# Kernel tuning notes

Hardware: AMD Instinct MI355X
Metric: run time of the kernel (lower is better)

## Reference

```python
import jax, jax.numpy as jnp
import numpy as np

HEADS, DIM_HEAD, BLOCK, EPS = 16, 64, 16, 1e-8


def _hattn(x, w_qkv, w_out, b_out):
    b, n, dim = x.shape
    h, dh, bsz = HEADS, DIM_HEAD, BLOCK
    scale = dh ** -0.5
    # n is a power of two, so the module's pad-to-pow2 step is a no-op.
    qkv = x @ w_qkv  # [b, n, 3*h*dh]
    q, k, v = jnp.split(qkv, 3, axis=-1)

    def to_heads(t):  # [b, n, h*dh] -> [(b h), n, dh]
        return t.reshape(b, n, h, dh).transpose(0, 2, 1, 3).reshape(b * h, n, dh)

    q, k, v = to_heads(q) * scale, to_heads(k), to_heads(v)

    num_levels = int(np.log2(n // bsz)) - 1
    levels = [(q, k, v)]
    for _ in range(num_levels):  # coarsen: mean-pool q,k; sum-pool v (mask=None path)
        q = q.reshape(b * h, -1, 2, dh).mean(axis=2)
        k = k.reshape(b * h, -1, 2, dh).mean(axis=2)
        v = v.reshape(b * h, -1, 2, dh).sum(axis=2)
        levels.append((q, k, v))

    def flip_blocks(t):  # swap adjacent blocks along the block axis: [B, nb, z, d]
        B, nb, z, d = t.shape
        return t.reshape(B, nb // 2, 2, z, d)[:, :, ::-1].reshape(B, nb, z, d)

    Ys = []
    last = len(levels) - 1
    for ind, (ql, kl, vl) in enumerate(reversed(levels)):  # coarsest -> finest
        B, N, d = ql.shape
        qb = ql.reshape(B, N // bsz, bsz, d)
        kb = vb = None
        kb = kl.reshape(B, N // bsz, bsz, d)
        vb = vl.reshape(B, N // bsz, bsz, d)
        if ind != last:  # off-diagonal pairing at coarse levels
            kb, vb = flip_blocks(kb), flip_blocks(vb)
        S = jnp.einsum('bnid,bnjd->bnij', qb, kb)
        S = S - S.max(axis=-1, keepdims=True)
        A = jnp.exp(S)
        y = jnp.einsum('bnij,bnjd->bnid', A, vb)
        Ys.append((y.reshape(B, N, d), A.sum(-1).reshape(B, N)))

    Y, Asum = Ys[0]
    for y_l, a_l in Ys[1:]:  # upsample-and-accumulate across levels
        Y = jnp.repeat(Y, 2, axis=1) + y_l
        Asum = jnp.repeat(Asum, 2, axis=1) + a_l

    out = Y / (Asum + EPS)[..., None]  # [(b h), n, dh]
    out = out.reshape(b, h, n, dh).transpose(0, 2, 1, 3).reshape(b, n, h * dh)
    return out @ w_out + b_out


def setup_inputs() -> dict:
    key = jax.random.key(0)
    k1, k2, k3 = jax.random.split(key, 3)
    b, n, dim = 4, 8192, 1024
    inner = HEADS * DIM_HEAD
    x = jax.random.normal(k1, (b, n, dim), dtype=jnp.float32)
    w_qkv = jax.random.normal(k2, (dim, inner * 3), dtype=jnp.float32) * 0.02
    w_out = jax.random.normal(k3, (inner, dim), dtype=jnp.float32) * 0.02
    b_out = jnp.zeros((dim,), dtype=jnp.float32)
    return {"x": x, "w_qkv": w_qkv, "w_out": w_out, "b_out": b_out}


def reference(x, w_qkv, w_out, b_out):
    return _hattn(x, w_qkv, w_out, b_out)
```

## Files before the change

### kernel.cpp

```cpp
#include <hip/hip_runtime.h>

typedef unsigned short u16;
typedef unsigned int u32;
typedef __bf16 bf16x8 __attribute__((ext_vector_type(8)));
typedef float f32x4 __attribute__((ext_vector_type(4)));

__device__ inline float bf2f(u16 u) { u32 x = ((u32)u) << 16; return __uint_as_float(x); }
__device__ inline u16 f2bf(float f) {
  u32 x = __float_as_uint(f);
  u32 r = (x + 0x7FFFu + ((x >> 16) & 1u)) >> 16;
  return (u16)r;
}
__device__ inline u32 pack2(float lo, float hi) {
  return (u32)f2bf(lo) | ((u32)f2bf(hi) << 16);
}

__global__ __launch_bounds__(256) void cast_bf16(const float* __restrict__ s,
                                                 u16* __restrict__ d, int n4) {
  const float4* s4 = (const float4*)s;
  u32* d2 = (u32*)d;
  int i = blockIdx.x * 256 + threadIdx.x;
  int stride = gridDim.x * 256;
  for (; i < n4; i += stride) {
    float4 f = s4[i];
    d2[2 * i]     = pack2(f.x, f.y);
    d2[2 * i + 1] = pack2(f.z, f.w);
  }
}

__global__ __launch_bounds__(256) void transpose_cast(const float* __restrict__ src,
                                                      u16* __restrict__ dst, int R, int C) {
  __shared__ float tile[32][33];
  int bx = blockIdx.x, by = blockIdx.y;
  int tx = threadIdx.x & 31, ty = threadIdx.x >> 5;
  for (int rr = ty; rr < 32; rr += 8)
    tile[rr][tx] = src[(size_t)(by * 32 + rr) * C + bx * 32 + tx];
  __syncthreads();
  for (int rr = ty; rr < 32; rr += 8)
    dst[(size_t)(bx * 32 + rr) * R + by * 32 + tx] = f2bf(tile[tx][rr]);
}

#define MFMAQ(AF, BF, MO, NO)                                                     \
  _Pragma("unroll") for (int mf = 0; mf < 4; ++mf)                                \
  _Pragma("unroll") for (int nf = 0; nf < 2; ++nf)                                \
  _Pragma("unroll") for (int kq = 0; kq < 2; ++kq)                                \
    acc[(MO) + mf][(NO) + nf] = __builtin_amdgcn_mfma_f32_16x16x32_bf16(          \
        AF[mf][kq], BF[nf][kq], acc[(MO) + mf][(NO) + nf], 0, 0, 0);

#define PH_OPEN12                                                                 \
  asm volatile("s_waitcnt lgkmcnt(8)" ::: "memory");                              \
  __builtin_amdgcn_s_barrier();                                                   \
  asm volatile("s_waitcnt lgkmcnt(0)" ::: "memory");                              \
  __builtin_amdgcn_sched_barrier(0);                                              \
  __builtin_amdgcn_s_setprio(1);

#define PH_OPEN                                                                   \
  __builtin_amdgcn_s_barrier();                                                   \
  asm volatile("s_waitcnt lgkmcnt(0)" ::: "memory");                              \
  __builtin_amdgcn_sched_barrier(0);                                              \
  __builtin_amdgcn_s_setprio(1);

#define PH_CLOSE                                                                  \
  __builtin_amdgcn_s_setprio(0);                                                  \
  __builtin_amdgcn_s_barrier();                                                   \
  __builtin_amdgcn_sched_barrier(0);

#define PH_CLOSE_VM                                                               \
  __builtin_amdgcn_s_setprio(0);                                                  \
  asm volatile("s_waitcnt vmcnt(4)" ::: "memory");                                \
  __builtin_amdgcn_s_barrier();                                                   \
  __builtin_amdgcn_sched_barrier(0);

template <int EPI>
__global__ __launch_bounds__(512, 2) void gemm8p(
    const u16* __restrict__ A, const u16* __restrict__ Bt, int M, int N, int K, int NB,
    u16* __restrict__ q0, u16* __restrict__ k0, u16* __restrict__ v0,
    u16* __restrict__ q4, u16* __restrict__ k4, u16* __restrict__ v4,
    float* __restrict__ out, const float* __restrict__ bias) {
  __shared__ u16 lds[2][2][16384];
  const int tid = threadIdx.x;
  const int lane = tid & 63;
  const int wave = tid >> 6;
  const int wm = wave >> 2, wn = wave & 3;
  const int lr = lane & 15, lg = lane >> 4;

  const int nwg = gridDim.x;
  const int bid = blockIdx.x;
  const int swz = (bid & 7) * (nwg >> 3) + (bid >> 3);
  const int m0 = (swz / NB) * 256;
  const int n0 = (swz % NB) * 256;
  const int NT = K >> 6;
  const int NI = NT >> 1;

  auto stage_half = [&](int buf, int ht, int kt_) {
    const u16* src = (ht < 2) ? A : Bt;
    const int r0 = (ht < 2) ? m0 : n0;
    u16* ldsop = &lds[buf][ht >> 1][0];
#pragma unroll
    for (int ii = 0; ii < 2; ++ii) {
      int c2 = ((ht & 1) * 2 + ii) * 512 + tid;
      int row = c2 >> 3, ps = c2 & 7;
      int ks = ps ^ (row & 7);
      const u16* g = src + (size_t)(r0 + row) * K + kt_ + ks * 8;
      char* l = (char*)ldsop + (size_t)((((ht & 1) * 2 + ii) * 512 + (tid & ~63)) * 16);
      __builtin_amdgcn_global_load_lds((const __attribute__((address_space(1))) void*)g,
                                       (__attribute__((address_space(3))) void*)l, 16, 0, 0);
    }
  };
  auto rdA = [&](int c, int mf, int kq) -> bf16x8 {
    int rl = wm * 128 + mf * 16 + lr;
    int sl = (kq * 4 + lg) ^ (rl & 7);
    return *(const bf16x8*)(&lds[c][0][rl * 64 + sl * 8]);
  };
  auto rdB = [&](int c, int nf, int kq) -> bf16x8 {
    int rl = wn * 64 + nf * 16 + lr;
    int sl = (kq * 4 + lg) ^ (rl & 7);
    return *(const bf16x8*)(&lds[c][1][rl * 64 + sl * 8]);
  };

  f32x4 acc[8][4];
#pragma unroll
  for (int mf = 0; mf < 8; ++mf)
#pragma unroll
    for (int nf = 0; nf < 4; ++nf) acc[mf][nf] = f32x4{0.f, 0.f, 0.f, 0.f};

  stage_half(0, 2, 0); stage_half(0, 3, 0); stage_half(0, 0, 0); stage_half(0, 1, 0);
  stage_half(1, 2, 64); stage_half(1, 3, 64);
  asm volatile("s_waitcnt vmcnt(4)" ::: "memory");
  __builtin_amdgcn_s_barrier();
  __builtin_amdgcn_sched_barrier(0);

  bf16x8 afA[4][2], afB[4][2], bA[2][2], bB[2][2];
  for (int it = 0; it < NI; ++it) {
    const int kO  = (2 * it + 1) << 6;
    const int t2  = 2 * it + 2, t3 = 2 * it + 3;
    const int kE2 = ((t2 < NT) ? t2 : NT - 1) << 6;
    const int kO2 = ((t3 < NT) ? t3 : NT - 1) << 6;

#pragma unroll
    for (int mf = 0; mf < 4; ++mf) { afA[mf][0] = rdA(0, mf, 0); afA[mf][1] = rdA(0, mf, 1); }
#pragma unroll
    for (int nf = 0; nf < 2; ++nf) { bA[nf][0] = rdB(0, nf, 0); bA[nf][1] = rdB(0, nf, 1); }
    stage_half(1, 0, kO);
    PH_OPEN12 MFMAQ(afA, bA, 0, 0) PH_CLOSE
#pragma unroll
    for (int nf = 0; nf < 2; ++nf) { bB[nf][0] = rdB(0, 2 + nf, 0); bB[nf][1] = rdB(0, 2 + nf, 1); }
    stage_half(1, 1, kO);
    PH_OPEN MFMAQ(afA, bB, 0, 2) PH_CLOSE
#pragma unroll
    for (int mf = 0; mf < 4; ++mf) { afB[mf][0] = rdA(0, 4 + mf, 0); afB[mf][1] = rdA(0, 4 + mf, 1); }
    stage_half(0, 2, kE2);
    PH_OPEN MFMAQ(afB, bB, 4, 2) PH_CLOSE
    stage_half(0, 3, kE2);
    PH_OPEN MFMAQ(afB, bA, 4, 0) PH_CLOSE_VM
#pragma unroll
    for (int mf = 0; mf < 4; ++mf) { afA[mf][0] = rdA(1, mf, 0); afA[mf][1] = rdA(1, mf, 1); }
#pragma unroll
    for (int nf = 0; nf < 2; ++nf) { bA[nf][0] = rdB(1, nf, 0); bA[nf][1] = rdB(1, nf, 1); }
    stage_half(0, 0, kE2);
    PH_OPEN12 MFMAQ(afA, bA, 0, 0) PH_CLOSE
#pragma unroll
    for (int nf = 0; nf < 2; ++nf) { bB[nf][0] = rdB(1, 2 + nf, 0); bB[nf][1] = rdB(1, 2 + nf, 1); }
    stage_half(0, 1, kE2);
    PH_OPEN MFMAQ(afA, bB, 0, 2) PH_CLOSE
#pragma unroll
    for (int mf = 0; mf < 4; ++mf) { afB[mf][0] = rdA(1, 4 + mf, 0); afB[mf][1] = rdA(1, 4 + mf, 1); }
    stage_half(1, 2, kO2);
    PH_OPEN MFMAQ(afB, bB, 4, 2) PH_CLOSE
    stage_half(1, 3, kO2);
    PH_OPEN MFMAQ(afB, bA, 4, 0) PH_CLOSE_VM
  }
  asm volatile("s_waitcnt vmcnt(0)" ::: "memory");

#pragma unroll
  for (int mf = 0; mf < 8; ++mf) {
#pragma unroll
    for (int nf = 0; nf < 4; ++nf) {
      int col = n0 + wn * 64 + nf * 16 + lr;
      if (EPI == 0) {
        int p = col >> 10, cc = col & 1023;
        int h = cc >> 6, d = cc & 63;
        u16* dst = (p == 0) ? q0 : (p == 1) ? k0 : v0;
        float sc = (p == 0) ? 0.125f : 1.0f;
#pragma unroll
        for (int jj = 0; jj < 4; ++jj) {
          int row = m0 + wm * 128 + mf * 16 + lg * 4 + jj;
          int b = row >> 13, nn = row & 8191;
          dst[((size_t)((b << 4) + h) * 8192 + nn) * 64 + d] = f2bf(acc[mf][nf][jj] * sc);
        }
        float s4 = acc[mf][nf][0] + acc[mf][nf][1] + acc[mf][nf][2] + acc[mf][nf][3];
        s4 += __shfl_xor(s4, 16);
        s4 += __shfl_xor(s4, 32);
        if (lane < 16) {
          int row = m0 + wm * 128 + mf * 16;
          int b = row >> 13, n4 = (row & 8191) >> 4;
          u16* dst4 = (p == 0) ? q4 : (p == 1) ? k4 : v4;
          float val = (p == 2) ? s4 : s4 * 0.0625f;
          if (p == 0) val *= 0.125f;
          dst4[((size_t)((b << 4) + h) * 512 + n4) * 64 + d] = f2bf(val);
        }
      } else {
        float bv = bias[col];
#pragma unroll
        for (int jj = 0; jj < 4; ++jj) {
          int row = m0 + wm * 128 + mf * 16 + lg * 4 + jj;
          out[(size_t)row * N + col] = acc[mf][nf][jj] + bv;
        }
      }
    }
  }
}

__global__ __launch_bounds__(256) void pool_level(
    const u16* __restrict__ qs, const u16* __restrict__ ks, const u16* __restrict__ vs,
    u16* __restrict__ qd, u16* __restrict__ kd, u16* __restrict__ vd, int P) {
  int t = blockIdx.x * 256 + threadIdx.x;
  if (t >= P) return;
  int a = blockIdx.y;
  const u32* s = (const u32*)(a == 0 ? qs : a == 1 ? ks : vs);
  u32* d = (u32*)(a == 0 ? qd : a == 1 ? kd : vd);
  int row = t >> 5, dp = t & 31;
  u32 u0 = s[(size_t)(2 * row) * 32 + dp];
  u32 u1 = s[(size_t)(2 * row + 1) * 32 + dp];
  float x0 = bf2f((u16)u0), x1 = bf2f((u16)(u0 >> 16));
  float y0 = bf2f((u16)u1), y1 = bf2f((u16)(u1 >> 16));
  float sc = (a == 2) ? 1.0f : 0.5f;
  d[t] = pack2((x0 + y0) * sc, (x1 + y1) * sc);
}

__global__ __launch_bounds__(256) void hattn_level(
    const u16* __restrict__ q, const u16* __restrict__ k, const u16* __restrict__ v,
    const float* __restrict__ pY, const float* __restrict__ pA,
    float* __restrict__ Ycur, float* __restrict__ Acur, int N) {
  __shared__ float qs[16][68], ks[16][68], vs[16][68];
  __shared__ float As[16][17];
  const int tid = threadIdx.x;
  const int jb = blockIdx.x;
  const int Bi = blockIdx.y;
  const int jk = jb ^ 1;
  const u32* qg = (const u32*)(q + ((size_t)Bi * N + jb * 16) * 64);
  const u32* kg = (const u32*)(k + ((size_t)Bi * N + jk * 16) * 64);
  const u32* vg = (const u32*)(v + ((size_t)Bi * N + jk * 16) * 64);
#pragma unroll
  for (int u = tid; u < 512; u += 256) {
    int row = u >> 5, dp = (u & 31) * 2;
    u32 a = qg[u]; qs[row][dp] = bf2f((u16)a); qs[row][dp + 1] = bf2f((u16)(a >> 16));
    u32 b = kg[u]; ks[row][dp] = bf2f((u16)b); ks[row][dp + 1] = bf2f((u16)(b >> 16));
    u32 c = vg[u]; vs[row][dp] = bf2f((u16)c); vs[row][dp + 1] = bf2f((u16)(c >> 16));
  }
  __syncthreads();
  const int i = tid >> 4, j = tid & 15;
  float s = 0.f;
  const float4* qv = (const float4*)&qs[i][0];
  const float4* kv = (const float4*)&ks[j][0];
#pragma unroll
  for (int d4 = 0; d4 < 16; ++d4) {
    float4 a = qv[d4], b = kv[d4];
    s += a.x * b.x + a.y * b.y + a.z * b.z + a.w * b.w;
  }
  float mx = s;
#pragma unroll
  for (int off = 8; off; off >>= 1) mx = fmaxf(mx, __shfl_xor(mx, off, 16));
  float aexp = __expf(s - mx);
  float asum = aexp;
#pragma unroll
  for (int off = 8; off; off >>= 1) asum += __shfl_xor(asum, off, 16);
  As[i][j] = aexp;
  __syncthreads();
  float y0 = 0, y1 = 0, y2 = 0, y3 = 0;
  const int d0 = j * 4;
#pragma unroll
  for (int jj = 0; jj < 16; ++jj) {
    float av = As[i][jj];
    const float4 vv = *(const float4*)&vs[jj][d0];
    y0 += av * vv.x; y1 += av * vv.y; y2 += av * vv.z; y3 += av * vv.w;
  }
  const int nf = jb * 16 + i;
  float at = asum;
  if (pY) {
    const float* py = pY + ((size_t)Bi * (N >> 1) + (nf >> 1)) * 64 + d0;
    y0 += py[0]; y1 += py[1]; y2 += py[2]; y3 += py[3];
    at += pA[(size_t)Bi * (N >> 1) + (nf >> 1)];
  }
  float* yo = Ycur + ((size_t)Bi * N + nf) * 64 + d0;
  yo[0] = y0; yo[1] = y1; yo[2] = y2; yo[3] = y3;
  if (j == 0) Acur[(size_t)Bi * N + nf] = at;
}

union F8 { u32 w[4]; bf16x8 v; };

__device__ inline void acc_row8(const u16* p, float* a) {
  const u32* qw = (const u32*)p;
#pragma unroll
  for (int m = 0; m < 4; ++m) {
    u32 u = qw[m];
    a[2 * m]     += bf2f((u16)u);
    a[2 * m + 1] += bf2f((u16)(u >> 16));
  }
}
__device__ inline bf16x8 mk8(const float* a, float s) {
  F8 f;
#pragma unroll
  for (int m = 0; m < 4; ++m) f.w[m] = pack2(a[2 * m] * s, a[2 * m + 1] * s);
  return f.v;
}
__device__ inline bf16x8 pool_frag(const u16* arr, int row0, int cnt, int slotq, float scale) {
  float a[8] = {0, 0, 0, 0, 0, 0, 0, 0};
  for (int m = 0; m < cnt; ++m) {
    int r = row0 + m;
    acc_row8(arr + r * 64 + ((slotq ^ (r & 7)) * 8), a);
  }
  return mk8(a, scale);
}
__device__ inline bf16x8 rd_frag(const u16* arr, int r, int slotq) {
  return *(const bf16x8*)(arr + r * 64 + ((slotq ^ (r & 7)) * 8));
}
template <int LVL>
__device__ inline bf16x8 vt_frag(const u16* Vt, int c, int rbase) {
  float a[8] = {0, 0, 0, 0, 0, 0, 0, 0};
  const u32* p = (const u32*)(Vt + c * 264 + rbase);
#pragma unroll
  for (int g = 0; g < (1 << LVL); ++g) {
#pragma unroll
    for (int m = 0; m < 4; ++m) {
      u32 u = p[g * 4 + m];
      int t = g * 8 + 2 * m;
      a[t >> LVL]       += bf2f((u16)u);
      a[(t + 1) >> LVL] += bf2f((u16)(u >> 16));
    }
  }
  return mk8(a, 1.0f);
}

__device__ inline bf16x8 qk_softmax(bf16x8 ka0, bf16x8 ka1, bf16x8 qb0, bf16x8 qb1,
                                    int lane, float* asum_out) {
  f32x4 s = {0.f, 0.f, 0.f, 0.f};
  s = __builtin_amdgcn_mfma_f32_16x16x32_bf16(ka0, qb0, s, 0, 0, 0);
  s = __builtin_amdgcn_mfma_f32_16x16x32_bf16(ka1, qb1, s, 0, 0, 0);
  float mx = fmaxf(fmaxf(s[0], s[1]), fmaxf(s[2], s[3]));
  mx = fmaxf(mx, __shfl_xor(mx, 32));
  mx = fmaxf(mx, __shfl_xor(mx, 16));
  float p0 = __expf(s[0] - mx), p1 = __expf(s[1] - mx);
  float p2 = __expf(s[2] - mx), p3 = __expf(s[3] - mx);
  float as = p0 + p1 + p2 + p3;
  as += __shfl_xor(as, 32);
  as += __shfl_xor(as, 16);
  *asum_out = as;
  u32 pk01 = pack2(p0, p1), pk23 = pack2(p2, p3);
  int jq = lane & 15, lg = lane >> 4;
  int a1 = ((((lg * 2) * 16) + jq) & 63) << 2;
  int a2 = ((((lg * 2 + 1) * 16) + jq) & 63) << 2;
  F8 f;
  f.w[0] = (u32)__builtin_amdgcn_ds_bpermute(a1, (int)pk01);
  f.w[1] = (u32)__builtin_amdgcn_ds_bpermute(a1, (int)pk23);
  f.w[2] = (u32)__builtin_amdgcn_ds_bpermute(a2, (int)pk01);
  f.w[3] = (u32)__builtin_amdgcn_ds_bpermute(a2, (int)pk23);
  if (lg >= 2) { f.w[0] = 0; f.w[1] = 0; f.w[2] = 0; f.w[3] = 0; }
  return f.v;
}

__global__ __launch_bounds__(512, 1) void attn_fine(
    const u16* __restrict__ q, const u16* __restrict__ k, const u16* __restrict__ v,
    const float* __restrict__ Y4, const float* __restrict__ A4,
    u16* __restrict__ outA) {
  __shared__ u16 Qs[16384];
  __shared__ u16 Ks[16384];
  __shared__ u16 Vt[16896];
  __shared__ float Yc1[128][68];
  __shared__ float Yc2[64][68];
  __shared__ float Yc3[32][68];
  __shared__ float SUMc[224];
  const int tid = threadIdx.x;
  const int lane = tid & 63;
  const int wv = tid >> 6;
  const int j = lane & 15, lg = lane >> 4;
  const int ci = blockIdx.x, Bi = blockIdx.y;
  const size_t gbase = ((size_t)Bi * 8192 + (size_t)ci * 256) * 64;

#pragma unroll
  for (int it = 0; it < 4; ++it) {
    int sidx = it * 512 + tid;
    int row = sidx >> 3, ps = sidx & 7;
    int ks_ = ps ^ (row & 7);
    const u16* gq = q + gbase + (size_t)row * 64 + ks_ * 8;
    const u16* gk = k + gbase + (size_t)row * 64 + ks_ * 8;
    char* lq = (char*)Qs + (size_t)(it * 512 + (tid & ~63)) * 16;
    char* lk = (char*)Ks + (size_t)(it * 512 + (tid & ~63)) * 16;
    __builtin_amdgcn_global_load_lds((const __attribute__((address_space(1))) void*)gq,
                                     (__attribute__((address_space(3))) void*)lq, 16, 0, 0);
    __builtin_amdgcn_global_load_lds((const __attribute__((address_space(1))) void*)gk,
                                     (__attribute__((address_space(3))) void*)lk, 16, 0, 0);
  }
  {
    const uint4* gv = (const uint4*)(v + gbase);
    u32* Vt32 = (u32*)Vt;
#pragma unroll
    for (int it = 0; it < 2; ++it) {
      int i = it * 512 + tid;
      int r2 = i >> 3, cg = i & 7, c0 = cg * 8;
      uint4 a = gv[(size_t)(2 * r2) * 8 + cg];
      uint4 b = gv[(size_t)(2 * r2 + 1) * 8 + cg];
      const u16* pa = (const u16*)&a;
      const u16* pb = (const u16*)&b;
#pragma unroll
      for (int m = 0; m < 8; ++m)
        Vt32[(c0 + m) * 132 + r2] = (u32)pa[m] | ((u32)pb[m] << 16);
    }
  }
  __syncthreads();

  {
    int kb = wv ^ 1;
    bf16x8 ka0 = pool_frag(Ks, kb * 32 + 2 * j, 2, lg, 0.5f);
    bf16x8 ka1 = pool_frag(Ks, kb * 32 + 2 * j, 2, 4 + lg, 0.5f);
    bf16x8 qb0 = pool_frag(Qs, wv * 32 + 2 * j, 2, lg, 0.5f);
    bf16x8 qb1 = pool_frag(Qs, wv * 32 + 2 * j, 2, 4 + lg, 0.5f);
    float as;
    bf16x8 pa = qk_softmax(ka0, ka1, qb0, qb1, lane, &as);
    if (lg == 0) SUMc[wv * 16 + j] = as;
    int rb = kb * 32 + (lg & 1) * 16;
    f32x4 acc[4];
#pragma unroll
    for (int ch = 0; ch < 4; ++ch) {
      bf16x8 vb = vt_frag<1>(Vt, ch * 16 + j, rb);
      acc[ch] = __builtin_amdgcn_mfma_f32_16x16x32_bf16(pa, vb, f32x4{0.f,0.f,0.f,0.f}, 0, 0, 0);
    }
#pragma unroll
    for (int ch = 0; ch < 4; ++ch)
#pragma unroll
      for (int jj = 0; jj < 4; ++jj)
        Yc1[wv * 16 + lg * 4 + jj][ch * 16 + j] = acc[ch][jj];
  }
  if (wv < 4) {
    int kb = wv ^ 1;
    bf16x8 ka0 = pool_frag(Ks, kb * 64 + 4 * j, 4, lg, 0.25f);
    bf16x8 ka1 = pool_frag(Ks, kb * 64 + 4 * j, 4, 4 + lg, 0.25f);
    bf16x8 qb0 = pool_frag(Qs, wv * 64 + 4 * j, 4, lg, 0.25f);
    bf16x8 qb1 = pool_frag(Qs, wv * 64 + 4 * j, 4, 4 + lg, 0.25f);
    float as;
    bf16x8 pa = qk_softmax(ka0, ka1, qb0, qb1, lane, &as);
    if (lg == 0) SUMc[128 + wv * 16 + j] = as;
    int rb = kb * 64 + (lg & 1) * 32;
    f32x4 acc[4];
#pragma unroll
    for (int ch = 0; ch < 4; ++ch) {
      bf16x8 vb = vt_frag<2>(Vt, ch * 16 + j, rb);
      acc[ch] = __builtin_amdgcn_mfma_f32_16x16x32_bf16(pa, vb, f32x4{0.f,0.f,0.f,0.f}, 0, 0, 0);
    }
#pragma unroll
    for (int ch = 0; ch < 4; ++ch)
#pragma unroll
      for (int jj = 0; jj < 4; ++jj)
        Yc2[wv * 16 + lg * 4 + jj][ch * 16 + j] = acc[ch][jj];
  }
  if (wv >= 6) {
    int w3 = wv - 6;
    int kb = w3 ^ 1;
    bf16x8 ka0 = pool_frag(Ks, kb * 128 + 8 * j, 8, lg, 0.125f);
    bf16x8 ka1 = pool_frag(Ks, kb * 128 + 8 * j, 8, 4 + lg, 0.125f);
    bf16x8 qb0 = pool_frag(Qs, w3 * 128 + 8 * j, 8, lg, 0.125f);
    bf16x8 qb1 = pool_frag(Qs, w3 * 128 + 8 * j, 8, 4 + lg, 0.125f);
    float as;
    bf16x8 pa = qk_softmax(ka0, ka1, qb0, qb1, lane, &as);
    if (lg == 0) SUMc[192 + w3 * 16 + j] = as;
    int rb = kb * 128 + (lg & 1) * 64;
    f32x4 acc[4];
#pragma unroll
    for (int ch = 0; ch < 4; ++ch) {
      bf16x8 vb = vt_frag<3>(Vt, ch * 16 + j, rb);
      acc[ch] = __builtin_amdgcn_mfma_f32_16x16x32_bf16(pa, vb, f32x4{0.f,0.f,0.f,0.f}, 0, 0, 0);
    }
#pragma unroll
    for (int ch = 0; ch < 4; ++ch)
#pragma unroll
      for (int jj = 0; jj < 4; ++jj)
        Yc3[w3 * 16 + lg * 4 + jj][ch * 16 + j] = acc[ch][jj];
  }
  __syncthreads();

  const int batch = Bi >> 4, h = Bi & 15;
#pragma unroll
  for (int bb = 0; bb < 2; ++bb) {
    int b = wv * 2 + bb;
    bf16x8 ka0 = rd_frag(Ks, b * 16 + j, lg);
    bf16x8 ka1 = rd_frag(Ks, b * 16 + j, 4 + lg);
    bf16x8 qb0 = rd_frag(Qs, b * 16 + j, lg);
    bf16x8 qb1 = rd_frag(Qs, b * 16 + j, 4 + lg);
    float as;
    bf16x8 pa = qk_softmax(ka0, ka1, qb0, qb1, lane, &as);
    float av[4];
#pragma unroll
    for (int jj = 0; jj < 4; ++jj)
      av[jj] = __int_as_float(__builtin_amdgcn_ds_bpermute((lg * 4 + jj) << 2,
                                                           __float_as_int(as)));
    int rb = b * 16 + (lg & 1) * 8;
    f32x4 acc[4];
#pragma unroll
    for (int ch = 0; ch < 4; ++ch) {
      bf16x8 vb = *(const bf16x8*)(Vt + (ch * 16 + j) * 264 + rb);
      acc[ch] = __builtin_amdgcn_mfma_f32_16x16x32_bf16(pa, vb, f32x4{0.f,0.f,0.f,0.f}, 0, 0, 0);
    }
    const size_t Y4row = (size_t)Bi * 512 + ci * 16 + b;
    float a4 = A4[Y4row];
    float y4v[4];
#pragma unroll
    for (int ch = 0; ch < 4; ++ch) y4v[ch] = Y4[Y4row * 64 + ch * 16 + j];
#pragma unroll
    for (int jj = 0; jj < 4; ++jj) {
      int r0 = b * 16 + lg * 4 + jj;
      float at = av[jj] + SUMc[r0 >> 1] + SUMc[128 + (r0 >> 2)] + SUMc[192 + (r0 >> 3)] + a4;
      float inv = 1.0f / (at + 1e-8f);
      size_t n = (size_t)ci * 256 + r0;
      u16* orow = outA + ((size_t)batch * 8192 + n) * 1024 + h * 64 + j;
#pragma unroll
      for (int ch = 0; ch < 4; ++ch) {
        float yt = acc[ch][jj] + Yc1[r0 >> 1][ch * 16 + j] + Yc2[r0 >> 2][ch * 16 + j] +
                   Yc3[r0 >> 3][ch * 16 + j] + y4v[ch];
        orow[ch * 16] = f2bf(yt * inv);
      }
    }
  }
}

extern "C" void kernel_launch(void* const* d_in, const int* in_sizes, int n_in,
                              void* d_out, int out_size, void* d_ws, size_t ws_size,
                              hipStream_t stream) {
  const float* x = (const float*)d_in[0];
  const float* w_qkv = (const float*)d_in[1];
  const float* w_out = (const float*)d_in[2];
  const float* b_out = (const float*)d_in[3];
  float* out = (float*)d_out;

  char* ws = (char*)d_ws;
  size_t off = 0;
  auto alloc = [&](size_t bytes) -> char* {
    char* p = ws + off;
    off += (bytes + 255) & ~(size_t)255;
    return p;
  };
  u16* xb = (u16*)alloc(33554432ull * 2);
  u16* wqkvT = (u16*)alloc(3072ull * 1024 * 2);
  u16* woutT = (u16*)alloc(1024ull * 1024 * 2);
  u16* q0 = (u16*)alloc(67108864ull);
  u16* k0 = (u16*)alloc(67108864ull);
  u16* v0 = (u16*)alloc(67108864ull);
  u16* qc = (u16*)alloc(8388608ull);
  u16* kc = (u16*)alloc(8388608ull);
  u16* vc = (u16*)alloc(8388608ull);
  float* Ybuf[2];
  Ybuf[0] = (float*)alloc(8388608ull);
  Ybuf[1] = (float*)alloc(8388608ull);
  float* Abuf[2];
  Abuf[0] = (float*)alloc(131072ull);
  Abuf[1] = (float*)alloc(131072ull);
  (void)ws_size; (void)in_sizes; (void)n_in; (void)out_size;

  cast_bf16<<<2048, 256, 0, stream>>>(x, xb, 33554432 / 4);
  transpose_cast<<<dim3(3072 / 32, 1024 / 32), 256, 0, stream>>>(w_qkv, wqkvT, 1024, 3072);
  transpose_cast<<<dim3(1024 / 32, 1024 / 32), 256, 0, stream>>>(w_out, woutT, 1024, 1024);

  const u16 *ql[9], *kl[9], *vl[9];
  ql[0] = q0; kl[0] = k0; vl[0] = v0;
  size_t co = 0;
  for (int l = 4; l <= 8; ++l) {
    ql[l] = qc + co; kl[l] = kc + co; vl[l] = vc + co;
    co += (size_t)64 * (8192 >> l) * 64;
  }

  gemm8p<0><<<1536, 512, 0, stream>>>(xb, wqkvT, 32768, 3072, 1024, 12,
                                      q0, k0, v0,
                                      (u16*)ql[4], (u16*)kl[4], (u16*)vl[4],
                                      nullptr, nullptr);

  for (int l = 5; l <= 8; ++l) {
    int Nl = 8192 >> l;
    int P = 64 * Nl * 32;
    pool_level<<<dim3((P + 255) / 256, 3), 256, 0, stream>>>(
        ql[l - 1], kl[l - 1], vl[l - 1], (u16*)ql[l], (u16*)kl[l], (u16*)vl[l], P);
  }
  for (int l = 8; l >= 4; --l) {
    int Nl = 8192 >> l;
    const float* pY = (l == 8) ? nullptr : Ybuf[(l + 1) & 1];
    const float* pA = (l == 8) ? nullptr : Abuf[(l + 1) & 1];
    hattn_level<<<dim3(Nl / 16, 64), 256, 0, stream>>>(
        ql[l], kl[l], vl[l], pY, pA, Ybuf[l & 1], Abuf[l & 1], Nl);
  }
  attn_fine<<<dim3(32, 64), 512, 0, stream>>>(q0, k0, v0, Ybuf[0], Abuf[0], xb);

  gemm8p<1><<<512, 512, 0, stream>>>(xb, woutT, 32768, 1024, 1024, 4,
                                     nullptr, nullptr, nullptr,
                                     nullptr, nullptr, nullptr, out, b_out);
}
```

Measured before the change: 473.1 us.

## Triple-buffer A tiles in GEMM and fuse coarse hierarchy into two launches

The GEMM main loop now processes one k-tile per iteration, with a three-deep LDS ring for A and a double buffer for B, and waits on vmcnt(8) so more loads stay in flight. The per-level pooling and coarse attention launches become one pooling kernel that builds every level from level 4, and one coarse-attention kernel that writes per-level outputs. attn_fine sums these outputs directly instead of reading an upsampled cascade. This removes serialized small launches and intermediate accumulation, at the cost of more LDS and extra reads in attn_fine.

```diff
diff --git a/kernel.cpp b/kernel.cpp
--- a/kernel.cpp
+++ b/kernel.cpp
@@ -65,9 +65,9 @@
   __builtin_amdgcn_s_barrier();                                                   \
   __builtin_amdgcn_sched_barrier(0);
 
-#define PH_CLOSE_VM                                                               \
+#define PH_CLOSE_VM8                                                              \
   __builtin_amdgcn_s_setprio(0);                                                  \
-  asm volatile("s_waitcnt vmcnt(4)" ::: "memory");                                \
+  asm volatile("s_waitcnt vmcnt(8)" ::: "memory");                                \
   __builtin_amdgcn_s_barrier();                                                   \
   __builtin_amdgcn_sched_barrier(0);
 
@@ -77,7 +77,8 @@
     u16* __restrict__ q0, u16* __restrict__ k0, u16* __restrict__ v0,
     u16* __restrict__ q4, u16* __restrict__ k4, u16* __restrict__ v4,
     float* __restrict__ out, const float* __restrict__ bias) {
-  __shared__ u16 lds[2][2][16384];
+  __shared__ u16 ldsA[3][16384];
+  __shared__ u16 ldsB[2][16384];
   const int tid = threadIdx.x;
   const int lane = tid & 63;
   const int wave = tid >> 6;
@@ -90,32 +91,28 @@
   const int m0 = (swz / NB) * 256;
   const int n0 = (swz % NB) * 256;
   const int NT = K >> 6;
-  const int NI = NT >> 1;
-
-  auto stage_half = [&](int buf, int ht, int kt_) {
-    const u16* src = (ht < 2) ? A : Bt;
-    const int r0 = (ht < 2) ? m0 : n0;
-    u16* ldsop = &lds[buf][ht >> 1][0];
+
+  auto stage_half = [&](u16* ldsop, const u16* src, int r0, int hb, int kt_) {
 #pragma unroll
     for (int ii = 0; ii < 2; ++ii) {
-      int c2 = ((ht & 1) * 2 + ii) * 512 + tid;
+      int c2 = (hb * 2 + ii) * 512 + tid;
       int row = c2 >> 3, ps = c2 & 7;
       int ks = ps ^ (row & 7);
       const u16* g = src + (size_t)(r0 + row) * K + kt_ + ks * 8;
-      char* l = (char*)ldsop + (size_t)((((ht & 1) * 2 + ii) * 512 + (tid & ~63)) * 16);
+      char* l = (char*)ldsop + (size_t)(((hb * 2 + ii) * 512 + (tid & ~63)) * 16);
       __builtin_amdgcn_global_load_lds((const __attribute__((address_space(1))) void*)g,
                                        (__attribute__((address_space(3))) void*)l, 16, 0, 0);
     }
   };
-  auto rdA = [&](int c, int mf, int kq) -> bf16x8 {
+  auto rdA = [&](const u16* Ab, int mf, int kq) -> bf16x8 {
     int rl = wm * 128 + mf * 16 + lr;
     int sl = (kq * 4 + lg) ^ (rl & 7);
-    return *(const bf16x8*)(&lds[c][0][rl * 64 + sl * 8]);
+    return *(const bf16x8*)(Ab + rl * 64 + sl * 8);
   };
-  auto rdB = [&](int c, int nf, int kq) -> bf16x8 {
+  auto rdB = [&](const u16* Bb, int nf, int kq) -> bf16x8 {
     int rl = wn * 64 + nf * 16 + lr;
     int sl = (kq * 4 + lg) ^ (rl & 7);
-    return *(const bf16x8*)(&lds[c][1][rl * 64 + sl * 8]);
+    return *(const bf16x8*)(Bb + rl * 64 + sl * 8);
   };
 
   f32x4 acc[8][4];
@@ -124,51 +121,39 @@
 #pragma unroll
     for (int nf = 0; nf < 4; ++nf) acc[mf][nf] = f32x4{0.f, 0.f, 0.f, 0.f};
 
-  stage_half(0, 2, 0); stage_half(0, 3, 0); stage_half(0, 0, 0); stage_half(0, 1, 0);
-  stage_half(1, 2, 64); stage_half(1, 3, 64);
-  asm volatile("s_waitcnt vmcnt(4)" ::: "memory");
+  stage_half(ldsA[0], A, m0, 0, 0); stage_half(ldsA[0], A, m0, 1, 0);
+  stage_half(ldsB[0], Bt, n0, 0, 0); stage_half(ldsB[0], Bt, n0, 1, 0);
+  const int k1 = ((NT > 1) ? 1 : 0) << 6;
+  stage_half(ldsA[1], A, m0, 0, k1); stage_half(ldsA[1], A, m0, 1, k1);
+  stage_half(ldsB[1], Bt, n0, 0, k1); stage_half(ldsB[1], Bt, n0, 1, k1);
+  asm volatile("s_waitcnt vmcnt(8)" ::: "memory");
   __builtin_amdgcn_s_barrier();
   __builtin_amdgcn_sched_barrier(0);
 
-  bf16x8 afA[4][2], afB[4][2], bA[2][2], bB[2][2];
-  for (int it = 0; it < NI; ++it) {
-    const int kO  = (2 * it + 1) << 6;
-    const int t2  = 2 * it + 2, t3 = 2 * it + 3;
-    const int kE2 = ((t2 < NT) ? t2 : NT - 1) << 6;
-    const int kO2 = ((t3 < NT) ? t3 : NT - 1) << 6;
-
-#pragma unroll
-    for (int mf = 0; mf < 4; ++mf) { afA[mf][0] = rdA(0, mf, 0); afA[mf][1] = rdA(0, mf, 1); }
-#pragma unroll
-    for (int nf = 0; nf < 2; ++nf) { bA[nf][0] = rdB(0, nf, 0); bA[nf][1] = rdB(0, nf, 1); }
-    stage_half(1, 0, kO);
+  for (int t = 0; t < NT; ++t) {
+    const u16* Ab = ldsA[t % 3];
+    const u16* Bb = ldsB[t & 1];
+    u16* A2 = ldsA[(t + 2) % 3];
+    u16* B2 = ldsB[t & 1];
+    const int k2 = (((t + 2) < NT) ? (t + 2) : (NT - 1)) << 6;
+
+    bf16x8 afA[4][2], afB[4][2], bA[2][2], bB[2][2];
+#pragma unroll
+    for (int mf = 0; mf < 4; ++mf) { afA[mf][0] = rdA(Ab, mf, 0); afA[mf][1] = rdA(Ab, mf, 1); }
+#pragma unroll
+    for (int nf = 0; nf < 2; ++nf) { bA[nf][0] = rdB(Bb, nf, 0); bA[nf][1] = rdB(Bb, nf, 1); }
+    stage_half(A2, A, m0, 0, k2);
     PH_OPEN12 MFMAQ(afA, bA, 0, 0) PH_CLOSE
 #pragma unroll
-    for (int nf = 0; nf < 2; ++nf) { bB[nf][0] = rdB(0, 2 + nf, 0); bB[nf][1] = rdB(0, 2 + nf, 1); }
-    stage_half(1, 1, kO);
+    for (int nf = 0; nf < 2; ++nf) { bB[nf][0] = rdB(Bb, 2 + nf, 0); bB[nf][1] = rdB(Bb, 2 + nf, 1); }
+    stage_half(A2, A, m0, 1, k2);
     PH_OPEN MFMAQ(afA, bB, 0, 2) PH_CLOSE
 #pragma unroll
-    for (int mf = 0; mf < 4; ++mf) { afB[mf][0] = rdA(0, 4 + mf, 0); afB[mf][1] = rdA(0, 4 + mf, 1); }
-    stage_half(0, 2, kE2);
+    for (int mf = 0; mf < 4; ++mf) { afB[mf][0] = rdA(Ab, 4 + mf, 0); afB[mf][1] = rdA(Ab, 4 + mf, 1); }
+    stage_half(B2, Bt, n0, 0, k2);
     PH_OPEN MFMAQ(afB, bB, 4, 2) PH_CLOSE
-    stage_half(0, 3, kE2);
-    PH_OPEN MFMAQ(afB, bA, 4, 0) PH_CLOSE_VM
-#pragma unroll
-    for (int mf = 0; mf < 4; ++mf) { afA[mf][0] = rdA(1, mf, 0); afA[mf][1] = rdA(1, mf, 1); }
-#pragma unroll
-    for (int nf = 0; nf < 2; ++nf) { bA[nf][0] = rdB(1, nf, 0); bA[nf][1] = rdB(1, nf, 1); }
-    stage_half(0, 0, kE2);
-    PH_OPEN12 MFMAQ(afA, bA, 0, 0) PH_CLOSE
-#pragma unroll
-    for (int nf = 0; nf < 2; ++nf) { bB[nf][0] = rdB(1, 2 + nf, 0); bB[nf][1] = rdB(1, 2 + nf, 1); }
-    stage_half(0, 1, kE2);
-    PH_OPEN MFMAQ(afA, bB, 0, 2) PH_CLOSE
-#pragma unroll
-    for (int mf = 0; mf < 4; ++mf) { afB[mf][0] = rdA(1, 4 + mf, 0); afB[mf][1] = rdA(1, 4 + mf, 1); }
-    stage_half(1, 2, kO2);
-    PH_OPEN MFMAQ(afB, bB, 4, 2) PH_CLOSE
-    stage_half(1, 3, kO2);
-    PH_OPEN MFMAQ(afB, bA, 4, 0) PH_CLOSE_VM
+    stage_half(B2, Bt, n0, 1, k2);
+    PH_OPEN MFMAQ(afB, bA, 4, 0) PH_CLOSE_VM8
   }
   asm volatile("s_waitcnt vmcnt(0)" ::: "memory");
 
@@ -211,36 +196,57 @@
   }
 }
 
-__global__ __launch_bounds__(256) void pool_level(
-    const u16* __restrict__ qs, const u16* __restrict__ ks, const u16* __restrict__ vs,
-    u16* __restrict__ qd, u16* __restrict__ kd, u16* __restrict__ vd, int P) {
+__global__ __launch_bounds__(256) void pool_all4(
+    const u16* __restrict__ q4, const u16* __restrict__ k4, const u16* __restrict__ v4,
+    u16* __restrict__ qd, u16* __restrict__ kd, u16* __restrict__ vd) {
   int t = blockIdx.x * 256 + threadIdx.x;
-  if (t >= P) return;
-  int a = blockIdx.y;
-  const u32* s = (const u32*)(a == 0 ? qs : a == 1 ? ks : vs);
-  u32* d = (u32*)(a == 0 ? qd : a == 1 ? kd : vd);
-  int row = t >> 5, dp = t & 31;
-  u32 u0 = s[(size_t)(2 * row) * 32 + dp];
-  u32 u1 = s[(size_t)(2 * row + 1) * 32 + dp];
-  float x0 = bf2f((u16)u0), x1 = bf2f((u16)(u0 >> 16));
-  float y0 = bf2f((u16)u1), y1 = bf2f((u16)(u1 >> 16));
-  float sc = (a == 2) ? 1.0f : 0.5f;
-  d[t] = pack2((x0 + y0) * sc, (x1 + y1) * sc);
-}
-
-__global__ __launch_bounds__(256) void hattn_level(
-    const u16* __restrict__ q, const u16* __restrict__ k, const u16* __restrict__ v,
-    const float* __restrict__ pY, const float* __restrict__ pA,
-    float* __restrict__ Ycur, float* __restrict__ Acur, int N) {
+  if (t >= 983040) return;
+  int arr = blockIdx.y;
+  int col = t & 31;
+  int rr = t >> 5;
+  int Bi = rr / 480;
+  int r = rr % 480;
+  int base, w, Nl;
+  if (r < 256)      { base = 0;   w = 2;  Nl = 256; }
+  else if (r < 384) { base = 256; w = 4;  Nl = 128; r -= 256; }
+  else if (r < 448) { base = 384; w = 8;  Nl = 64;  r -= 384; }
+  else              { base = 448; w = 16; Nl = 32;  r -= 448; }
+  const u32* s = (const u32*)(arr == 0 ? q4 : arr == 1 ? k4 : v4);
+  const u32* src = s + ((size_t)Bi * 512 + (size_t)r * w) * 32 + col;
+  float lo = 0, hi = 0;
+  for (int m = 0; m < w; ++m) {
+    u32 u = src[(size_t)m * 32];
+    lo += bf2f((u16)u); hi += bf2f((u16)(u >> 16));
+  }
+  float sc = (arr == 2) ? 1.0f : (1.0f / (float)w);
+  u32* d = (u32*)(arr == 0 ? qd : arr == 1 ? kd : vd);
+  d[(size_t)2048 * base + ((size_t)Bi * Nl + r) * 32 + col] = pack2(lo * sc, hi * sc);
+}
+
+__global__ __launch_bounds__(256) void hattn_coarse(
+    const u16* __restrict__ q4, const u16* __restrict__ k4, const u16* __restrict__ v4,
+    const u16* __restrict__ qc, const u16* __restrict__ kc, const u16* __restrict__ vc,
+    float* __restrict__ ylvl, float* __restrict__ alvl) {
   __shared__ float qs[16][68], ks[16][68], vs[16][68];
   __shared__ float As[16][17];
+  const int bx = blockIdx.x, Bi = blockIdx.y;
+  int lvl, jb;
+  if (bx < 32)      { lvl = 0; jb = bx; }
+  else if (bx < 48) { lvl = 1; jb = bx - 32; }
+  else if (bx < 56) { lvl = 2; jb = bx - 48; }
+  else if (bx < 60) { lvl = 3; jb = bx - 56; }
+  else              { lvl = 4; jb = bx - 60; }
+  const int N = 512 >> lvl;
+  const int srcb[5] = {0, 0, 256, 384, 448};
+  const int offr[5] = {0, 512, 768, 896, 960};
+  const u16* qp = (lvl == 0) ? q4 : qc + (size_t)4096 * srcb[lvl];
+  const u16* kp = (lvl == 0) ? k4 : kc + (size_t)4096 * srcb[lvl];
+  const u16* vp = (lvl == 0) ? v4 : vc + (size_t)4096 * srcb[lvl];
   const int tid = threadIdx.x;
-  const int jb = blockIdx.x;
-  const int Bi = blockIdx.y;
   const int jk = jb ^ 1;
-  const u32* qg = (const u32*)(q + ((size_t)Bi * N + jb * 16) * 64);
-  const u32* kg = (const u32*)(k + ((size_t)Bi * N + jk * 16) * 64);
-  const u32* vg = (const u32*)(v + ((size_t)Bi * N + jk * 16) * 64);
+  const u32* qg = (const u32*)(qp + ((size_t)Bi * N + jb * 16) * 64);
+  const u32* kg = (const u32*)(kp + ((size_t)Bi * N + jk * 16) * 64);
+  const u32* vg = (const u32*)(vp + ((size_t)Bi * N + jk * 16) * 64);
 #pragma unroll
   for (int u = tid; u < 512; u += 256) {
     int row = u >> 5, dp = (u & 31) * 2;
@@ -276,15 +282,9 @@
     y0 += av * vv.x; y1 += av * vv.y; y2 += av * vv.z; y3 += av * vv.w;
   }
   const int nf = jb * 16 + i;
-  float at = asum;
-  if (pY) {
-    const float* py = pY + ((size_t)Bi * (N >> 1) + (nf >> 1)) * 64 + d0;
-    y0 += py[0]; y1 += py[1]; y2 += py[2]; y3 += py[3];
-    at += pA[(size_t)Bi * (N >> 1) + (nf >> 1)];
-  }
-  float* yo = Ycur + ((size_t)Bi * N + nf) * 64 + d0;
+  float* yo = ylvl + (size_t)4096 * offr[lvl] + ((size_t)Bi * N + nf) * 64 + d0;
   yo[0] = y0; yo[1] = y1; yo[2] = y2; yo[3] = y3;
-  if (j == 0) Acur[(size_t)Bi * N + nf] = at;
+  if (j == 0) alvl[(size_t)64 * offr[lvl] + (size_t)Bi * N + nf] = asum;
 }
 
 union F8 { u32 w[4]; bf16x8 v; };
@@ -361,7 +361,7 @@
 
 __global__ __launch_bounds__(512, 1) void attn_fine(
     const u16* __restrict__ q, const u16* __restrict__ k, const u16* __restrict__ v,
-    const float* __restrict__ Y4, const float* __restrict__ A4,
+    const float* __restrict__ ylvl, const float* __restrict__ alvl,
     u16* __restrict__ outA) {
   __shared__ u16 Qs[16384];
   __shared__ u16 Ks[16384];
@@ -479,6 +479,7 @@
   __syncthreads();
 
   const int batch = Bi >> 4, h = Bi & 15;
+  const int offr[5] = {0, 512, 768, 896, 960};
 #pragma unroll
   for (int bb = 0; bb < 2; ++bb) {
     int b = wv * 2 + bb;
@@ -500,11 +501,18 @@
       bf16x8 vb = *(const bf16x8*)(Vt + (ch * 16 + j) * 264 + rb);
       acc[ch] = __builtin_amdgcn_mfma_f32_16x16x32_bf16(pa, vb, f32x4{0.f,0.f,0.f,0.f}, 0, 0, 0);
     }
-    const size_t Y4row = (size_t)Bi * 512 + ci * 16 + b;
-    float a4 = A4[Y4row];
-    float y4v[4];
-#pragma unroll
-    for (int ch = 0; ch < 4; ++ch) y4v[ch] = Y4[Y4row * 64 + ch * 16 + j];
+    const int i4 = ci * 16 + b;
+    float a4 = 0;
+    float y4v[4] = {0, 0, 0, 0};
+#pragma unroll
+    for (int l = 0; l < 5; ++l) {
+      int Rl = 512 >> l;
+      size_t idx = (size_t)Bi * Rl + (i4 >> l);
+      a4 += alvl[(size_t)64 * offr[l] + idx];
+      const float* yp = ylvl + (size_t)4096 * offr[l] + idx * 64;
+#pragma unroll
+      for (int ch = 0; ch < 4; ++ch) y4v[ch] += yp[ch * 16 + j];
+    }
 #pragma unroll
     for (int jj = 0; jj < 4; ++jj) {
       int r0 = b * 16 + lg * 4 + jj;
@@ -544,48 +552,26 @@
   u16* q0 = (u16*)alloc(67108864ull);
   u16* k0 = (u16*)alloc(67108864ull);
   u16* v0 = (u16*)alloc(67108864ull);
-  u16* qc = (u16*)alloc(8388608ull);
-  u16* kc = (u16*)alloc(8388608ull);
-  u16* vc = (u16*)alloc(8388608ull);
-  float* Ybuf[2];
-  Ybuf[0] = (float*)alloc(8388608ull);
-  Ybuf[1] = (float*)alloc(8388608ull);
-  float* Abuf[2];
-  Abuf[0] = (float*)alloc(131072ull);
-  Abuf[1] = (float*)alloc(131072ull);
+  u16* q4 = (u16*)alloc(4194304ull);
+  u16* k4 = (u16*)alloc(4194304ull);
+  u16* v4 = (u16*)alloc(4194304ull);
+  u16* qc = (u16*)alloc(3932160ull);
+  u16* kc = (u16*)alloc(3932160ull);
+  u16* vc = (u16*)alloc(3932160ull);
+  float* ylvl = (float*)alloc(16252928ull);
+  float* alvl = (float*)alloc(253952ull);
   (void)ws_size; (void)in_sizes; (void)n_in; (void)out_size;
 
   cast_bf16<<<2048, 256, 0, stream>>>(x, xb, 33554432 / 4);
   transpose_cast<<<dim3(3072 / 32, 1024 / 32), 256, 0, stream>>>(w_qkv, wqkvT, 1024, 3072);
   transpose_cast<<<dim3(1024 / 32, 1024 / 32), 256, 0, stream>>>(w_out, woutT, 1024, 1024);
 
-  const u16 *ql[9], *kl[9], *vl[9];
-  ql[0] = q0; kl[0] = k0; vl[0] = v0;
-  size_t co = 0;
-  for (int l = 4; l <= 8; ++l) {
-    ql[l] = qc + co; kl[l] = kc + co; vl[l] = vc + co;
-    co += (size_t)64 * (8192 >> l) * 64;
-  }
-
   gemm8p<0><<<1536, 512, 0, stream>>>(xb, wqkvT, 32768, 3072, 1024, 12,
-                                      q0, k0, v0,
-                                      (u16*)ql[4], (u16*)kl[4], (u16*)vl[4],
-                                      nullptr, nullptr);
-
-  for (int l = 5; l <= 8; ++l) {
-    int Nl = 8192 >> l;
-    int P = 64 * Nl * 32;
-    pool_level<<<dim3((P + 255) / 256, 3), 256, 0, stream>>>(
-        ql[l - 1], kl[l - 1], vl[l - 1], (u16*)ql[l], (u16*)kl[l], (u16*)vl[l], P);
-  }
-  for (int l = 8; l >= 4; --l) {
-    int Nl = 8192 >> l;
-    const float* pY = (l == 8) ? nullptr : Ybuf[(l + 1) & 1];
-    const float* pA = (l == 8) ? nullptr : Abuf[(l + 1) & 1];
-    hattn_level<<<dim3(Nl / 16, 64), 256, 0, stream>>>(
-        ql[l], kl[l], vl[l], pY, pA, Ybuf[l & 1], Abuf[l & 1], Nl);
-  }
-  attn_fine<<<dim3(32, 64), 512, 0, stream>>>(q0, k0, v0, Ybuf[0], Abuf[0], xb);
+                                      q0, k0, v0, q4, k4, v4, nullptr, nullptr);
+
+  pool_all4<<<dim3(3840, 3), 256, 0, stream>>>(q4, k4, v4, qc, kc, vc);
+  hattn_coarse<<<dim3(62, 64), 256, 0, stream>>>(q4, k4, v4, qc, kc, vc, ylvl, alvl);
+  attn_fine<<<dim3(32, 64), 512, 0, stream>>>(q0, k0, v0, ylvl, alvl, xb);
 
   gemm8p<1><<<512, 512, 0, stream>>>(xb, woutT, 32768, 1024, 1024, 4,
                                      nullptr, nullptr, nullptr,
```

Result: slower. 495.5 us (+4.7%).
